# Optimization experiments

Hardware: AMD Instinct MI355X
Metric: run time of the kernel (lower is better)

## Reference

```python
import jax, jax.numpy as jnp
import numpy as np

RADIUS = 0.2
N_NEIGHBOR = 32


def setup_inputs() -> dict:
    key = jax.random.key(0)
    k1, k2 = jax.random.split(key)
    B, N, S = 8, 8192, 2048
    pos = jax.random.uniform(k1, (B, N, 3), dtype=jnp.float32)
    centroids = jax.random.randint(k2, (B, S), 0, N, dtype=jnp.int64)
    centroids_index = jnp.zeros((1,), dtype=jnp.int64)
    index_voxels = jnp.zeros((1,), dtype=jnp.int64)
    return {"pos": pos, "centroids": centroids,
            "centroids_index": centroids_index, "index_voxels": index_voxels}


def reference(pos, centroids, centroids_index, index_voxels):
    # pos: [B, N, 3]; centroids: [B, S] indices into N.
    B, N, _ = pos.shape
    # index_points: gather center coordinates -> [B, S, 3]
    center_pos = jnp.take_along_axis(pos, centroids[:, :, None], axis=1)
    # squared pairwise distances [B, S, N]: ||c||^2 + ||p||^2 - 2 c.p
    sqrdists = (jnp.sum(center_pos ** 2, axis=-1)[:, :, None]
                + jnp.sum(pos ** 2, axis=-1)[:, None, :]
                - 2.0 * jnp.einsum('bsd,bnd->bsn', center_pos, pos))
    # indices, with out-of-radius points set to sentinel N
    base = jnp.arange(N, dtype=jnp.int32)[None, None, :]
    group_idx = jnp.where(sqrdists > RADIUS ** 2, jnp.int32(N), base)
    # sort ascending and take first n_neighbor valid indices
    group_idx = jnp.sort(group_idx, axis=-1)[:, :, :N_NEIGHBOR]  # [B, S, K]
    # replace remaining sentinels with the first (closest-index) valid neighbor
    group_first = group_idx[:, :, :1]
    group_idx = jnp.where(group_idx == N, group_first, group_idx)
    return group_idx
```

## Files before the change

kernel.cpp:

```cpp
#include <hip/hip_runtime.h>

#define NPTS 8192
#define NQ   2048
#define NBATCH 8
#define KNN  32
#define R2   0.04f

__global__ __launch_bounds__(256)
void gg_prep(const float* __restrict__ pos, float4* __restrict__ pack, int total) {
    int i = blockIdx.x * blockDim.x + threadIdx.x;
    if (i >= total) return;
    float x = pos[i * 3 + 0];
    float y = pos[i * 3 + 1];
    float z = pos[i * 3 + 2];
    float n = __fadd_rn(__fadd_rn(__fmul_rn(x, x), __fmul_rn(y, y)), __fmul_rn(z, z));
    pack[i] = make_float4(x, y, z, n);
}

__global__ __launch_bounds__(256)
void gg_ballquery(const float4* __restrict__ pack,
                  const int* __restrict__ centroids,
                  int* __restrict__ out) {
    const int wid  = threadIdx.x >> 6;
    const int lane = threadIdx.x & 63;
    const int q    = blockIdx.x * 4 + wid;
    const int b    = q >> 11;

    const float4* __restrict__ pp = pack + b * NPTS;

    const int cidx = centroids[q];
    const float4 c = pp[cidx];
    const float cx = c.x, cy = c.y, cz = c.z, cn = c.w;

    int* __restrict__ oq = out + q * KNN;
    const unsigned long long below = (1ull << lane) - 1ull;

    int collected = 0;
    int first_idx = NPTS;

    float4 c0 = pp[lane];
    float4 c1 = pp[lane + 64];
    float4 c2 = pp[lane + 128];
    float4 c3 = pp[lane + 192];

    #pragma unroll 1
    for (int base = 0; base < NPTS; base += 256) {
        float4 p0 = c0, p1 = c1, p2 = c2, p3 = c3;
        if (base + 256 < NPTS) {
            c0 = pp[base + 256 + lane];
            c1 = pp[base + 320 + lane];
            c2 = pp[base + 384 + lane];
            c3 = pp[base + 448 + lane];
        }

        #pragma unroll
        for (int j = 0; j < 4; ++j) {
            float4 p = (j == 0) ? p0 : (j == 1) ? p1 : (j == 2) ? p2 : p3;
            float dot = __fadd_rn(__fadd_rn(__fmul_rn(cx, p.x), __fmul_rn(cy, p.y)),
                                  __fmul_rn(cz, p.z));
            float s   = __fsub_rn(__fadd_rn(cn, p.w), __fmul_rn(2.0f, dot));
            bool keep = !(s > R2);

            unsigned long long mask = __ballot(keep);
            if (mask) {
                int sub = base + j * 64;
                if (collected == 0) first_idx = sub + (int)__builtin_ctzll(mask);
                if (keep) {
                    int slot = collected + (int)__popcll(mask & below);
                    if (slot < KNN) oq[slot] = sub + lane;
                }
                collected += (int)__popcll(mask);
                if (collected >= KNN) goto done;
            }
        }
    }
done:

    if (collected < KNN) {
        int slot = collected + lane;
        if (slot < KNN) oq[slot] = first_idx;
    }
}

extern "C" void kernel_launch(void* const* d_in, const int* in_sizes, int n_in,
                              void* d_out, int out_size, void* d_ws, size_t ws_size,
                              hipStream_t stream) {
    const float* pos       = (const float*)d_in[0];
    const int*   centroids = (const int*)d_in[1];
    int*         out       = (int*)d_out;

    float4* pack = (float4*)d_ws;

    const int total = NBATCH * NPTS;
    gg_prep<<<dim3((total + 255) / 256), dim3(256), 0, stream>>>(pos, pack, total);

    const int nq = NBATCH * NQ;
    gg_ballquery<<<dim3(nq / 4), dim3(256), 0, stream>>>(pack, centroids, out);
}
```

Measured before the change: 82.02 us.

## Process two ball queries per wavefront to share point loads

Each wavefront now handles two centroid queries instead of one. Every point tile it loads is tested against both centers, which halves global and L2 point traffic per query and halves the number of waves launched. The per-lane prefix count now uses the mbcnt intrinsics instead of a popcount on a shifted mask. In exchange, a wave keeps looping until both queries have 32 neighbors, and the exit check only runs after each 256-point chunk rather than inside it, so a wave can do extra work for whichever query finishes first.

```diff
diff --git a/kernel.cpp b/kernel.cpp
--- a/kernel.cpp
+++ b/kernel.cpp
@@ -23,62 +23,88 @@
                   int* __restrict__ out) {
     const int wid  = threadIdx.x >> 6;
     const int lane = threadIdx.x & 63;
-    const int q    = blockIdx.x * 4 + wid;
-    const int b    = q >> 11;
+    const int w    = blockIdx.x * 4 + wid;
+    const int q0   = w * 2;
+    const int b    = q0 >> 11;
 
     const float4* __restrict__ pp = pack + b * NPTS;
 
-    const int cidx = centroids[q];
-    const float4 c = pp[cidx];
-    const float cx = c.x, cy = c.y, cz = c.z, cn = c.w;
+    const float4 ca = pp[centroids[q0]];
+    const float4 cb = pp[centroids[q0 + 1]];
 
-    int* __restrict__ oq = out + q * KNN;
-    const unsigned long long below = (1ull << lane) - 1ull;
+    int* __restrict__ oa = out + q0 * KNN;
+    int* __restrict__ ob = oa + KNN;
 
-    int collected = 0;
-    int first_idx = NPTS;
+    int colA = 0, colB = 0;
+    int firstA = NPTS, firstB = NPTS;
 
-    float4 c0 = pp[lane];
-    float4 c1 = pp[lane + 64];
-    float4 c2 = pp[lane + 128];
-    float4 c3 = pp[lane + 192];
+    float4 r0 = pp[lane];
+    float4 r1 = pp[lane + 64];
+    float4 r2 = pp[lane + 128];
+    float4 r3 = pp[lane + 192];
 
     #pragma unroll 1
     for (int base = 0; base < NPTS; base += 256) {
-        float4 p0 = c0, p1 = c1, p2 = c2, p3 = c3;
+        float4 p0 = r0, p1 = r1, p2 = r2, p3 = r3;
         if (base + 256 < NPTS) {
-            c0 = pp[base + 256 + lane];
-            c1 = pp[base + 320 + lane];
-            c2 = pp[base + 384 + lane];
-            c3 = pp[base + 448 + lane];
+            r0 = pp[base + 256 + lane];
+            r1 = pp[base + 320 + lane];
+            r2 = pp[base + 384 + lane];
+            r3 = pp[base + 448 + lane];
         }
 
         #pragma unroll
         for (int j = 0; j < 4; ++j) {
             float4 p = (j == 0) ? p0 : (j == 1) ? p1 : (j == 2) ? p2 : p3;
-            float dot = __fadd_rn(__fadd_rn(__fmul_rn(cx, p.x), __fmul_rn(cy, p.y)),
-                                  __fmul_rn(cz, p.z));
-            float s   = __fsub_rn(__fadd_rn(cn, p.w), __fmul_rn(2.0f, dot));
-            bool keep = !(s > R2);
+            const int sub = base + j * 64;
 
-            unsigned long long mask = __ballot(keep);
-            if (mask) {
-                int sub = base + j * 64;
-                if (collected == 0) first_idx = sub + (int)__builtin_ctzll(mask);
-                if (keep) {
-                    int slot = collected + (int)__popcll(mask & below);
-                    if (slot < KNN) oq[slot] = sub + lane;
+            if (colA < KNN) {
+                float dot = __fadd_rn(__fadd_rn(__fmul_rn(ca.x, p.x), __fmul_rn(ca.y, p.y)),
+                                      __fmul_rn(ca.z, p.z));
+                float s   = __fsub_rn(__fadd_rn(ca.w, p.w), __fmul_rn(2.0f, dot));
+                bool keep = !(s > R2);
+                unsigned long long mask = __ballot(keep);
+                if (mask) {
+                    if (colA == 0) firstA = sub + (int)__builtin_ctzll(mask);
+                    int prefix = (int)__builtin_amdgcn_mbcnt_hi(
+                        (unsigned)(mask >> 32),
+                        __builtin_amdgcn_mbcnt_lo((unsigned)mask, 0u));
+                    if (keep) {
+                        int slot = colA + prefix;
+                        if (slot < KNN) oa[slot] = sub + lane;
+                    }
+                    colA += (int)__popcll(mask);
                 }
-                collected += (int)__popcll(mask);
-                if (collected >= KNN) goto done;
+            }
+            if (colB < KNN) {
+                float dot = __fadd_rn(__fadd_rn(__fmul_rn(cb.x, p.x), __fmul_rn(cb.y, p.y)),
+                                      __fmul_rn(cb.z, p.z));
+                float s   = __fsub_rn(__fadd_rn(cb.w, p.w), __fmul_rn(2.0f, dot));
+                bool keep = !(s > R2);
+                unsigned long long mask = __ballot(keep);
+                if (mask) {
+                    if (colB == 0) firstB = sub + (int)__builtin_ctzll(mask);
+                    int prefix = (int)__builtin_amdgcn_mbcnt_hi(
+                        (unsigned)(mask >> 32),
+                        __builtin_amdgcn_mbcnt_lo((unsigned)mask, 0u));
+                    if (keep) {
+                        int slot = colB + prefix;
+                        if (slot < KNN) ob[slot] = sub + lane;
+                    }
+                    colB += (int)__popcll(mask);
+                }
             }
         }
+        if (colA >= KNN && colB >= KNN) break;
     }
-done:
 
-    if (collected < KNN) {
-        int slot = collected + lane;
-        if (slot < KNN) oq[slot] = first_idx;
+    if (colA < KNN) {
+        int slot = colA + lane;
+        if (slot < KNN) oa[slot] = firstA;
+    }
+    if (colB < KNN) {
+        int slot = colB + lane;
+        if (slot < KNN) ob[slot] = firstB;
     }
 }
 
@@ -94,6 +120,6 @@
     const int total = NBATCH * NPTS;
     gg_prep<<<dim3((total + 255) / 256), dim3(256), 0, stream>>>(pos, pack, total);
 
-    const int nq = NBATCH * NQ;
-    gg_ballquery<<<dim3(nq / 4), dim3(256), 0, stream>>>(pack, centroids, out);
+    const int nw = (NBATCH * NQ) / 2;
+    gg_ballquery<<<dim3(nw / 4), dim3(256), 0, stream>>>(pack, centroids, out);
 }
```

Measured after the change: 79.06 us. -3.6%, faster.
